# Kernel optimization log

Measured on AMD Instinct MI355X. Metric: run time of the kernel, lower is better.

The kernel has to match this reference:

```python
import jax, jax.numpy as jnp
import numpy as np
from jax.ops import segment_sum

N_NODES = 100000
IN_CH = 128
HIDDEN = 256
N_EDGES = 1600000


def setup_inputs() -> dict:
    key = jax.random.key(0)
    ks = jax.random.split(key, 8)
    x = jax.random.normal(ks[0], (N_NODES, IN_CH), dtype=jnp.float32)
    edge_index = jax.random.randint(ks[1], (2, N_EDGES), 0, N_NODES, dtype=jnp.int64)
    edges = jax.random.randint(ks[2], (N_EDGES, 2), 0, N_NODES, dtype=jnp.int64)
    s1 = 1.0 / np.sqrt(IN_CH)
    s2 = 1.0 / np.sqrt(HIDDEN)
    W1l = jax.random.normal(ks[3], (IN_CH, HIDDEN), dtype=jnp.float32) * s1
    W1r = jax.random.normal(ks[4], (IN_CH, HIDDEN), dtype=jnp.float32) * s1
    b1 = jnp.zeros((HIDDEN,), dtype=jnp.float32)
    W2l = jax.random.normal(ks[5], (HIDDEN, HIDDEN), dtype=jnp.float32) * s2
    W2r = jax.random.normal(ks[6], (HIDDEN, HIDDEN), dtype=jnp.float32) * s2
    b2 = jnp.zeros((HIDDEN,), dtype=jnp.float32)
    return {"x": x, "edge_index": edge_index, "edges": edges,
            "W1l": W1l, "b1": b1, "W1r": W1r,
            "W2l": W2l, "b2": b2, "W2r": W2r}


def _sage_conv(x, src, dst, Wl, b, Wr, n_nodes):
    # PyG SAGEConv (aggr='mean'): out = lin_l(mean_{j in N(i)} x_j) + lin_r(x_i)
    msg_sum = segment_sum(x[src], dst, num_segments=n_nodes)        # [N, F]
    deg = segment_sum(jnp.ones((src.shape[0],), x.dtype), dst, num_segments=n_nodes)
    mean = msg_sum / jnp.maximum(deg, 1.0)[:, None]                 # zero-deg -> 0
    return mean @ Wl + b + x @ Wr


def reference(x, edge_index, edges, W1l, b1, W1r, W2l, b2, W2r):
    src, dst = edge_index[0], edge_index[1]
    n = x.shape[0]
    h = jax.nn.relu(_sage_conv(x, src, dst, W1l, b1, W1r, n))
    z = _sage_conv(h, src, dst, W2l, b2, W2r, n)                    # [N, hidden]
    # decode: dot product over candidate edge pairs
    return jnp.sum(z[edges[:, 0]] * z[edges[:, 1]], axis=-1)        # [E2]
```

## Files before the change

### kernel.cpp

```cpp
#include <hip/hip_runtime.h>

#define IN_CH 128
#define HID   256
#define PB_VT 16
#define BCAP  6144

typedef __attribute__((ext_vector_type(8))) short bf16x8;
typedef __attribute__((ext_vector_type(4))) float f32x4;
typedef __attribute__((ext_vector_type(2))) float f32x2;
typedef __attribute__((ext_vector_type(8))) unsigned short ushort8;

__device__ __forceinline__ ushort f2b(float f) {
    unsigned u = __float_as_uint(f);
    unsigned r = (u + 0x7fffu + ((u >> 16) & 1u)) >> 16;
    return (ushort)r;
}
__device__ __forceinline__ float b2f(ushort h) {
    return __uint_as_float(((unsigned)h) << 16);
}
__device__ __forceinline__ void fp8x8_to_f32(uint2 v, float f[8]) {
    f32x2 a = __builtin_amdgcn_cvt_pk_f32_fp8((int)v.x, false);
    f32x2 b = __builtin_amdgcn_cvt_pk_f32_fp8((int)v.x, true);
    f32x2 c = __builtin_amdgcn_cvt_pk_f32_fp8((int)v.y, false);
    f32x2 d = __builtin_amdgcn_cvt_pk_f32_fp8((int)v.y, true);
    f[0] = a[0]; f[1] = a[1]; f[2] = b[0]; f[3] = b[1];
    f[4] = c[0]; f[5] = c[1]; f[6] = d[0]; f[7] = d[1];
}

__device__ __forceinline__ void prep_w_body(const float* __restrict__ Wl,
                                            const float* __restrict__ Wr,
                                            ushort* __restrict__ Wt,
                                            int KH, bool permK, int idx) {
    int ktot = 2 * KH;
    if (idx >= 256 * ktot) return;
    int n = idx / ktot, k = idx % ktot;
    int kh = (k < KH) ? k : (k - KH);
    int c = kh;
    if (permK) {
        int j = kh & 63;
        c = (kh & ~63) | ((j & 3) * 16 + (j >> 2));
    }
    float v = (k < KH) ? Wl[(size_t)c * 256 + n] : Wr[(size_t)c * 256 + n];
    Wt[idx] = f2b(v);
}

__global__ __launch_bounds__(256)
void fused_cvt_prep(const float* __restrict__ x, ushort* __restrict__ xb,
                    unsigned char* __restrict__ x8, int n4, int nCvt,
                    const float* __restrict__ W1l, const float* __restrict__ W1r, ushort* __restrict__ Wt1,
                    const float* __restrict__ W2l, const float* __restrict__ W2r, ushort* __restrict__ Wt2,
                    int* __restrict__ bucketCntG, int* __restrict__ bucketCntP) {
    int b = blockIdx.x;
    int t = threadIdx.x;
    if (b < nCvt) {
        int i = b * 256 + t;
        if (i < n4) {
            float4 v = ((const float4*)x)[i];
            ushort4 u;
            u.x = f2b(v.x); u.y = f2b(v.y); u.z = f2b(v.z); u.w = f2b(v.w);
            ((ushort4*)xb)[i] = u;
            int p = __builtin_amdgcn_cvt_pk_fp8_f32(v.x, v.y, 0, false);
            p = __builtin_amdgcn_cvt_pk_fp8_f32(v.z, v.w, p, true);
            ((unsigned*)x8)[i] = (unsigned)p;
        }
    } else if (b < nCvt + 256) {
        prep_w_body(W1l, W1r, Wt1, IN_CH, false, (b - nCvt) * 256 + t);
    } else if (b < nCvt + 256 + 512) {
        prep_w_body(W2l, W2r, Wt2, HID, true, (b - nCvt - 256) * 256 + t);
    } else {
        bucketCntG[t] = 0;
        bucketCntG[t + 256] = 0;
        bucketCntP[t] = 0;
        bucketCntP[t + 256] = 0;
    }
}

__global__ __launch_bounds__(256)
void scatter_reserve_kernel(const int* __restrict__ src, const int* __restrict__ dst,
                            const int* __restrict__ edges,
                            int* __restrict__ bucketCntG, int* __restrict__ bucketCntP,
                            unsigned* __restrict__ tmpG, unsigned long long* __restrict__ tmpP,
                            int E, int E2, int NBUK, int NBG) {
    __shared__ int hist[512];
    __shared__ int cur[512];
    int t = threadIdx.x;
    bool isG = (int)blockIdx.x < NBG;
    int blk = isG ? blockIdx.x : blockIdx.x - NBG;
    for (int i = t; i < NBUK; i += 256) hist[i] = 0;
    __syncthreads();
    long long e0 = (long long)blk * (256 * PB_VT);
    if (isG) {
#pragma unroll
        for (int i = 0; i < PB_VT; i++) {
            long long e = e0 + i * 256 + t;
            if (e < E) atomicAdd(&hist[dst[e] >> 8], 1);
        }
    } else {
#pragma unroll
        for (int i = 0; i < PB_VT; i++) {
            long long e = e0 + i * 256 + t;
            if (e < E2) atomicAdd(&hist[edges[e * 2] >> 8], 1);
        }
    }
    __syncthreads();
    int* bcnt = isG ? bucketCntG : bucketCntP;
    for (int i = t; i < NBUK; i += 256) {
        int hc = hist[i];
        cur[i] = (hc > 0) ? atomicAdd(&bcnt[i], hc) : 0;
    }
    __syncthreads();
    if (isG) {
#pragma unroll
        for (int i = 0; i < PB_VT; i++) {
            long long e = e0 + i * 256 + t;
            if (e < E) {
                int d = dst[e];
                int bk = d >> 8;
                int pos = atomicAdd(&cur[bk], 1);
                tmpG[(size_t)bk * BCAP + pos] = ((unsigned)src[e] << 8) | (unsigned)(d & 255);
            }
        }
    } else {
#pragma unroll
        for (int i = 0; i < PB_VT; i++) {
            long long e = e0 + i * 256 + t;
            if (e < E2) {
                int2 ab = *(const int2*)(edges + e * 2);
                int bk = ab.x >> 8;
                int pos = atomicAdd(&cur[bk], 1);
                tmpP[(size_t)bk * BCAP + pos] = ((unsigned long long)(unsigned)(ab.x & 255) << 56)
                                              | ((unsigned long long)(unsigned)ab.y << 32)
                                              | (unsigned)e;
            }
        }
    }
}

__global__ __launch_bounds__(256)
void bucket_sort_kernel(const unsigned* __restrict__ tmpG, const unsigned long long* __restrict__ tmpP,
                        const int* __restrict__ bucketCntG, const int* __restrict__ bucketCntP,
                        int* __restrict__ count, int* __restrict__ offs,
                        int* __restrict__ nbr, unsigned long long* __restrict__ pairs,
                        int N, int Npad, int NBUK) {
    __shared__ int h[256], loffs[256], lcur[256];
    int t = threadIdx.x;
    bool isG = (int)blockIdx.x < NBUK;
    int b = isG ? blockIdx.x : blockIdx.x - NBUK;
    int s = b * BCAP;
    int c = isG ? bucketCntG[b] : bucketCntP[b];
    h[t] = 0;
    __syncthreads();
    if (isG) {
        for (int i = t; i < c; i += 256) atomicAdd(&h[tmpG[s + i] & 255], 1);
    } else {
        for (int i = t; i < c; i += 256) atomicAdd(&h[(int)(tmpP[s + i] >> 56)], 1);
    }
    __syncthreads();
    int v = h[t];
    loffs[t] = v;
    __syncthreads();
    for (int d = 1; d < 256; d <<= 1) {
        int u = (t >= d) ? loffs[t - d] : 0;
        __syncthreads(); loffs[t] += u; __syncthreads();
    }
    int excl = loffs[t] - v;
    lcur[t] = excl;
    int node = b * 256 + t;
    if (node < N) {
        int base = isG ? 0 : Npad;
        count[base + node] = v;
        offs[base + node] = s + excl;
    }
    __syncthreads();
    if (isG) {
        for (int i = t; i < c; i += 256) {
            unsigned w = tmpG[s + i];
            int p = atomicAdd(&lcur[w & 255], 1);
            nbr[s + p] = (int)(w >> 8);
        }
    } else {
        for (int i = t; i < c; i += 256) {
            unsigned long long w = tmpP[s + i];
            int p = atomicAdd(&lcur[(int)(w >> 56)], 1);
            pairs[s + p] = w & 0x00FFFFFFFFFFFFFFull;
        }
    }
}

__global__ void agg1_kernel(const unsigned char* __restrict__ x8, const int* __restrict__ nbr,
                            const int* __restrict__ offs, const int* __restrict__ count,
                            ushort* __restrict__ agg, int N) {
    int w = blockIdx.x * 4 + (threadIdx.x >> 6);
    if (w >= N) return;
    int lane = threadIdx.x & 63;
    int grp = lane >> 4, gl = lane & 15;
    int start = offs[w], cnt = count[w];
    float a0[8], a1[8];
#pragma unroll
    for (int i = 0; i < 8; i++) { a0[i] = 0.0f; a1[i] = 0.0f; }
    int j = grp;
    for (; j + 4 < cnt; j += 8) {
        int s0 = nbr[start + j];
        int s1 = nbr[start + j + 4];
        uint2 v0 = *(const uint2*)(x8 + (size_t)s0 * IN_CH + gl * 8);
        uint2 v1 = *(const uint2*)(x8 + (size_t)s1 * IN_CH + gl * 8);
        float f0[8], f1[8];
        fp8x8_to_f32(v0, f0); fp8x8_to_f32(v1, f1);
#pragma unroll
        for (int i = 0; i < 8; i++) { a0[i] += f0[i]; a1[i] += f1[i]; }
    }
    if (j < cnt) {
        int s0 = nbr[start + j];
        uint2 v0 = *(const uint2*)(x8 + (size_t)s0 * IN_CH + gl * 8);
        float f0[8];
        fp8x8_to_f32(v0, f0);
#pragma unroll
        for (int i = 0; i < 8; i++) a0[i] += f0[i];
    }
#pragma unroll
    for (int i = 0; i < 8; i++) {
        a0[i] += a1[i];
        a0[i] += __shfl_xor(a0[i], 16, 64);
        a0[i] += __shfl_xor(a0[i], 32, 64);
    }
    if (grp == 0) {
        float r = 1.0f / fmaxf((float)cnt, 1.0f);
        ushort8 o;
#pragma unroll
        for (int i = 0; i < 8; i++) o[i] = f2b(a0[i] * r);
        *(ushort8*)(agg + (size_t)w * IN_CH + gl * 8) = o;
    }
}

__global__ void agg2_kernel(const unsigned char* __restrict__ h8, const int* __restrict__ nbr,
                            const int* __restrict__ offs, const int* __restrict__ count,
                            ushort* __restrict__ agg, int N) {
    int w = blockIdx.x * 4 + (threadIdx.x >> 6);
    if (w >= N) return;
    int lane = threadIdx.x & 63;
    int half = lane >> 5, hl = lane & 31;
    int start = offs[w], cnt = count[w];
    float a0[8], a1[8];
#pragma unroll
    for (int i = 0; i < 8; i++) { a0[i] = 0.0f; a1[i] = 0.0f; }
    int j = half;
    for (; j + 6 < cnt; j += 8) {
        int s0 = nbr[start + j];
        int s1 = nbr[start + j + 2];
        int s2 = nbr[start + j + 4];
        int s3 = nbr[start + j + 6];
        uint2 v0 = *(const uint2*)(h8 + (size_t)s0 * HID + hl * 8);
        uint2 v1 = *(const uint2*)(h8 + (size_t)s1 * HID + hl * 8);
        uint2 v2 = *(const uint2*)(h8 + (size_t)s2 * HID + hl * 8);
        uint2 v3 = *(const uint2*)(h8 + (size_t)s3 * HID + hl * 8);
        float f0[8], f1[8], f2[8], f3[8];
        fp8x8_to_f32(v0, f0); fp8x8_to_f32(v1, f1);
        fp8x8_to_f32(v2, f2); fp8x8_to_f32(v3, f3);
#pragma unroll
        for (int i = 0; i < 8; i++) {
            a0[i] += f0[i] + f2[i];
            a1[i] += f1[i] + f3[i];
        }
    }
    for (; j < cnt; j += 2) {
        int s0 = nbr[start + j];
        uint2 v0 = *(const uint2*)(h8 + (size_t)s0 * HID + hl * 8);
        float f0[8];
        fp8x8_to_f32(v0, f0);
#pragma unroll
        for (int i = 0; i < 8; i++) a0[i] += f0[i];
    }
#pragma unroll
    for (int i = 0; i < 8; i++) {
        a0[i] += a1[i];
        a0[i] += __shfl_xor(a0[i], 32, 64);
    }
    if (half == 0) {
        float r = 1.0f / fmaxf((float)cnt, 1.0f);
        ushort8 o;
#pragma unroll
        for (int i = 0; i < 8; i++) o[i] = f2b(a0[i] * r);
        *(ushort8*)(agg + (size_t)w * HID + hl * 8) = o;
    }
}

template<int KTOT, bool RELU, bool WBF16, bool WFP8>
__global__ __launch_bounds__(512, 4)
void sage_gemm_mfma(const ushort* __restrict__ Aleft, const ushort* __restrict__ Aright,
                    const ushort* __restrict__ Wt, const float* __restrict__ bias,
                    ushort* __restrict__ out, unsigned char* __restrict__ out8, int N) {
    constexpr int KH = KTOT / 2;
    __shared__ ushort smem[2048 + 8192];
    ushort* As = smem;
    ushort* Bs = smem + 2048;

    const int t = threadIdx.x;
    const int wave = t >> 6;
    const int lane = t & 63;
    const int quad = lane >> 4;
    const int l16  = lane & 15;
    const int rowBase = blockIdx.x * 64;

    const int aRow = t >> 3;
    const int aK   = (t & 7) * 4;
    const bool aRowOK = (rowBase + aRow) < N;
    const int aLds = ((aRow >> 4) * 64 + (aRow & 15) * 4 + (aK >> 3)) * 8 + (aK & 7);

    const int bN   = t >> 1;
    const int bCh0 = (t & 1) * 2;
    const int bFragBase = (bN >> 6) * 256 + ((bN >> 4) & 3) * 64 + (bN & 15) * 4;

    int bFrag[2];
#pragma unroll
    for (int nt = 0; nt < 2; nt++) {
        int c = wave * 32 + nt * 16 + l16;
        bFrag[nt] = ((c >> 6) * 256 + ((c >> 4) & 3) * 64 + (c & 15) * 4 + quad) * 8;
    }

    f32x4 acc[4][2];
#pragma unroll
    for (int i = 0; i < 4; i++)
#pragma unroll
        for (int j = 0; j < 2; j++) acc[i][j] = (f32x4)0.0f;

    unsigned long long aReg = 0ull;
    ulonglong2 bReg[2];
    if (aRowOK)
        aReg = *(const unsigned long long*)(Aleft + (size_t)(rowBase + aRow) * KH + aK);
    bReg[0] = *(const ulonglong2*)(Wt + (size_t)bN * KTOT + bCh0 * 8);
    bReg[1] = *(const ulonglong2*)(Wt + (size_t)bN * KTOT + (bCh0 + 1) * 8);

    for (int k0 = 0; k0 < KTOT; k0 += 32) {
        __syncthreads();
        *(unsigned long long*)&As[aLds] = aReg;
        *(ulonglong2*)&Bs[(bFragBase + bCh0) * 8]     = bReg[0];
        *(ulonglong2*)&Bs[(bFragBase + bCh0 + 1) * 8] = bReg[1];

        int kn = k0 + 32;
        if (kn < KTOT) {
            if (aRowOK) {
                const ushort* Ap = (kn < KH)
                    ? (Aleft  + (size_t)(rowBase + aRow) * KH + (kn + aK))
                    : (Aright + (size_t)(rowBase + aRow) * KH + (kn - KH + aK));
                aReg = *(const unsigned long long*)Ap;
            }
            bReg[0] = *(const ulonglong2*)(Wt + (size_t)bN * KTOT + kn + bCh0 * 8);
            bReg[1] = *(const ulonglong2*)(Wt + (size_t)bN * KTOT + kn + (bCh0 + 1) * 8);
        }
        __syncthreads();

        bf16x8 af[4], bf[2];
#pragma unroll
        for (int mt = 0; mt < 4; mt++)
            af[mt] = *(const bf16x8*)&As[(mt * 64 + l16 * 4 + quad) * 8];
#pragma unroll
        for (int nt = 0; nt < 2; nt++)
            bf[nt] = *(const bf16x8*)&Bs[bFrag[nt]];
#pragma unroll
        for (int mt = 0; mt < 4; mt++)
#pragma unroll
            for (int nt = 0; nt < 2; nt++)
                acc[mt][nt] = __builtin_amdgcn_mfma_f32_16x16x32_bf16(
                    af[mt], bf[nt], acc[mt][nt], 0, 0, 0);
    }

    float bv[2];
#pragma unroll
    for (int nt = 0; nt < 2; nt++) bv[nt] = bias[wave * 32 + nt * 16 + l16];
    ushort* tile = smem;

#pragma unroll
    for (int hf = 0; hf < 2; hf++) {
        __syncthreads();
#pragma unroll
        for (int mh = 0; mh < 2; mh++) {
            int mt = hf * 2 + mh;
#pragma unroll
            for (int reg = 0; reg < 4; reg++) {
                int rl = mh * 16 + quad * 4 + reg;
                float v0 = acc[mt][0][reg] + bv[0];
                float v1 = acc[mt][1][reg] + bv[1];
                if (RELU) { v0 = fmaxf(v0, 0.0f); v1 = fmaxf(v1, 0.0f); }
                ushort2 o;
                o.x = f2b(v0); o.y = f2b(v1);
                *(ushort2*)&tile[rl * 256 + (wave >> 1) * 64 + l16 * 4 + (wave & 1) * 2] = o;
            }
        }
        __syncthreads();
#pragma unroll
        for (int i = 0; i < 2; i++) {
            int ch = i * 512 + t;
            int rl = ch >> 5, c16 = ch & 31;
            int row = rowBase + hf * 32 + rl;
            if (row < N) {
                ushort8 w = *(const ushort8*)&tile[rl * 256 + c16 * 8];
                if (WBF16)
                    *(ushort8*)(out + (size_t)row * 256 + c16 * 8) = w;
                if (WFP8) {
                    int u0 = __builtin_amdgcn_cvt_pk_fp8_f32(b2f(w[0]), b2f(w[1]), 0, false);
                    u0 = __builtin_amdgcn_cvt_pk_fp8_f32(b2f(w[2]), b2f(w[3]), u0, true);
                    int u1 = __builtin_amdgcn_cvt_pk_fp8_f32(b2f(w[4]), b2f(w[5]), 0, false);
                    u1 = __builtin_amdgcn_cvt_pk_fp8_f32(b2f(w[6]), b2f(w[7]), u1, true);
                    uint2 o8;
                    o8.x = (unsigned)u0; o8.y = (unsigned)u1;
                    *(uint2*)(out8 + (size_t)row * 256 + c16 * 8) = o8;
                }
            }
        }
    }
}

__global__ void decode2_kernel(const unsigned char* __restrict__ z8,
                               const unsigned long long* __restrict__ pairs,
                               const int* __restrict__ offsA, const int* __restrict__ countA,
                               float* __restrict__ out, int N) {
    int a = blockIdx.x * 4 + (threadIdx.x >> 6);
    if (a >= N) return;
    int cnt = countA[a];
    if (cnt == 0) return;
    int lane = threadIdx.x & 63;
    int half = lane >> 5, hl = lane & 31;
    int start = offsA[a];

    float ar[8];
    {
        uint2 va = *(const uint2*)(z8 + (size_t)a * HID + hl * 8);
        fp8x8_to_f32(va, ar);
    }

    int j = half;
    for (; j + 6 < cnt; j += 8) {
        unsigned long long p0 = pairs[start + j];
        unsigned long long p1 = pairs[start + j + 2];
        unsigned long long p2 = pairs[start + j + 4];
        unsigned long long p3 = pairs[start + j + 6];
        int b0 = (int)((p0 >> 32) & 0xFFFFFFu), e0 = (int)(p0 & 0xffffffffu);
        int b1 = (int)((p1 >> 32) & 0xFFFFFFu), e1 = (int)(p1 & 0xffffffffu);
        int b2 = (int)((p2 >> 32) & 0xFFFFFFu), e2 = (int)(p2 & 0xffffffffu);
        int b3 = (int)((p3 >> 32) & 0xFFFFFFu), e3 = (int)(p3 & 0xffffffffu);
        uint2 v0 = *(const uint2*)(z8 + (size_t)b0 * HID + hl * 8);
        uint2 v1 = *(const uint2*)(z8 + (size_t)b1 * HID + hl * 8);
        uint2 v2 = *(const uint2*)(z8 + (size_t)b2 * HID + hl * 8);
        uint2 v3 = *(const uint2*)(z8 + (size_t)b3 * HID + hl * 8);
        float f0[8], f1[8], f2[8], f3[8];
        fp8x8_to_f32(v0, f0); fp8x8_to_f32(v1, f1);
        fp8x8_to_f32(v2, f2); fp8x8_to_f32(v3, f3);
        float s0 = 0.f, s1 = 0.f, s2 = 0.f, s3 = 0.f;
#pragma unroll
        for (int i = 0; i < 8; i++) {
            s0 = fmaf(ar[i], f0[i], s0);
            s1 = fmaf(ar[i], f1[i], s1);
            s2 = fmaf(ar[i], f2[i], s2);
            s3 = fmaf(ar[i], f3[i], s3);
        }
#pragma unroll
        for (int off = 1; off < 32; off <<= 1) {
            s0 += __shfl_xor(s0, off, 64);
            s1 += __shfl_xor(s1, off, 64);
            s2 += __shfl_xor(s2, off, 64);
            s3 += __shfl_xor(s3, off, 64);
        }
        if (hl == 0) { out[e0] = s0; out[e1] = s1; out[e2] = s2; out[e3] = s3; }
    }
    for (; j < cnt; j += 2) {
        unsigned long long p0 = pairs[start + j];
        int b0 = (int)((p0 >> 32) & 0xFFFFFFu), e0 = (int)(p0 & 0xffffffffu);
        uint2 v0 = *(const uint2*)(z8 + (size_t)b0 * HID + hl * 8);
        float f0[8];
        fp8x8_to_f32(v0, f0);
        float s0 = 0.f;
#pragma unroll
        for (int i = 0; i < 8; i++) s0 = fmaf(ar[i], f0[i], s0);
#pragma unroll
        for (int off = 1; off < 32; off <<= 1) s0 += __shfl_xor(s0, off, 64);
        if (hl == 0) out[e0] = s0;
    }
}

extern "C" void kernel_launch(void* const* d_in, const int* in_sizes, int n_in,
                              void* d_out, int out_size, void* d_ws, size_t ws_size,
                              hipStream_t stream) {
    const float* x    = (const float*)d_in[0];
    const int* eidx   = (const int*)d_in[1];
    const int* edges  = (const int*)d_in[2];
    const float* W1l  = (const float*)d_in[3];
    const float* b1   = (const float*)d_in[4];
    const float* W1r  = (const float*)d_in[5];
    const float* W2l  = (const float*)d_in[6];
    const float* b2   = (const float*)d_in[7];
    const float* W2r  = (const float*)d_in[8];
    float* out = (float*)d_out;

    const int N  = in_sizes[0] / IN_CH;
    const int E  = in_sizes[1] / 2;
    const int E2 = in_sizes[2] / 2;
    const int* src = eidx;
    const int* dst = eidx + E;

    const int NBUK = (N + 255) >> 8;
    const int Npad = NBUK << 8;
    const int NBG  = (E  + 256 * PB_VT - 1) / (256 * PB_VT);
    const int NBP  = (E2 + 256 * PB_VT - 1) / (256 * PB_VT);

    int* count      = (int*)d_ws;
    int* offs       = count + 2 * Npad;
    int* bucketCntG = offs + 2 * Npad;
    int* bucketCntP = bucketCntG + 512;
    int* nbr        = bucketCntP + 512;
    size_t intWords = (size_t)(nbr - (int*)d_ws) + (size_t)NBUK * BCAP;
    intWords = (intWords + 1) & ~(size_t)1;
    unsigned long long* pairs = (unsigned long long*)((int*)d_ws + intWords);
    ushort* xb    = (ushort*)(pairs + (size_t)NBUK * BCAP);
    ushort* agg1b = xb + (size_t)N * IN_CH;
    ushort* agg2b = xb;
    ushort* h     = agg1b + (size_t)N * IN_CH;
    unsigned char* h8 = (unsigned char*)(h + (size_t)N * HID);
    unsigned char* z8 = h8 + (size_t)N * HID;
    ushort* Wt1   = (ushort*)(z8 + (size_t)N * HID);
    ushort* Wt2   = Wt1 + 256 * 256;
    unsigned char* x8 = z8 + (size_t)N * HID / 2;
    unsigned* tmpG = (unsigned*)h8;
    unsigned long long* tmpP =
        (unsigned long long*)(tmpG + (((size_t)NBUK * BCAP + 1) & ~(size_t)1));

    int n4 = N * IN_CH / 4;
    int nCvt = (n4 + 255) / 256;
    fused_cvt_prep<<<nCvt + 256 + 512 + 1, 256, 0, stream>>>(
        x, xb, x8, n4, nCvt, W1l, W1r, Wt1, W2l, W2r, Wt2, bucketCntG, bucketCntP);

    scatter_reserve_kernel<<<NBG + NBP, 256, 0, stream>>>(
        src, dst, edges, bucketCntG, bucketCntP, tmpG, tmpP, E, E2, NBUK, NBG);
    bucket_sort_kernel<<<2 * NBUK, 256, 0, stream>>>(
        tmpG, tmpP, bucketCntG, bucketCntP, count, offs, nbr, pairs, N, Npad, NBUK);

    agg1_kernel<<<(N + 3) / 4, 256, 0, stream>>>(x8, nbr, offs, count, agg1b, N);
    sage_gemm_mfma<2 * IN_CH, true, true, true><<<(N + 63) / 64, 512, 0, stream>>>(
        agg1b, xb, Wt1, b1, h, h8, N);

    agg2_kernel<<<(N + 3) / 4, 256, 0, stream>>>(h8, nbr, offs, count, agg2b, N);
    sage_gemm_mfma<2 * HID, false, false, true><<<(N + 63) / 64, 512, 0, stream>>>(
        agg2b, h, Wt2, b2, h , z8, N);

    decode2_kernel<<<(N + 3) / 4, 256, 0, stream>>>(z8, pairs, offs + Npad, count + Npad, out, N);
}
```

Before: 527.0 us.

## Double-buffer LDS in SAGE GEMM and enlarge row tile to 128

The MFMA GEMM now stages A and B tiles in two LDS buffers, so the next K-slice is written while the current one is consumed. This removes one barrier per K step. Each block also covers 128 rows instead of 64, giving every wave 8x2 accumulator tiles; B fragments are reused over more rows and the grid is halved. The cost is more LDS (about 48KB) and more accumulator registers, which may reduce occupancy under launch_bounds(512,4). The epilogue loop is extended to write out four half-tiles.

Result: faster. 486.5 us (-7.7%).

```diff
diff --git a/kernel.cpp b/kernel.cpp
--- a/kernel.cpp
+++ b/kernel.cpp
@@ -290,21 +290,22 @@
                     const ushort* __restrict__ Wt, const float* __restrict__ bias,
                     ushort* __restrict__ out, unsigned char* __restrict__ out8, int N) {
     constexpr int KH = KTOT / 2;
-    __shared__ ushort smem[2048 + 8192];
-    ushort* As = smem;
-    ushort* Bs = smem + 2048;
+    constexpr int S  = KTOT / 32;
+    __shared__ ushort smem[2 * 4096 + 2 * 8192];
+    ushort* AsB[2] = { smem, smem + 4096 };
+    ushort* BsB[2] = { smem + 8192, smem + 16384 };
 
     const int t = threadIdx.x;
     const int wave = t >> 6;
     const int lane = t & 63;
     const int quad = lane >> 4;
     const int l16  = lane & 15;
-    const int rowBase = blockIdx.x * 64;
-
-    const int aRow = t >> 3;
-    const int aK   = (t & 7) * 4;
+    const int rowBase = blockIdx.x * 128;
+
+    const int aRow = t >> 2;
+    const int aCh  = t & 3;
     const bool aRowOK = (rowBase + aRow) < N;
-    const int aLds = ((aRow >> 4) * 64 + (aRow & 15) * 4 + (aK >> 3)) * 8 + (aK & 7);
+    const int aLds = ((aRow >> 4) * 64 + (aRow & 15) * 4 + aCh) * 8;
 
     const int bN   = t >> 1;
     const int bCh0 = (t & 1) * 2;
@@ -317,51 +318,57 @@
         bFrag[nt] = ((c >> 6) * 256 + ((c >> 4) & 3) * 64 + (c & 15) * 4 + quad) * 8;
     }
 
-    f32x4 acc[4][2];
-#pragma unroll
-    for (int i = 0; i < 4; i++)
+    f32x4 acc[8][2];
+#pragma unroll
+    for (int i = 0; i < 8; i++)
 #pragma unroll
         for (int j = 0; j < 2; j++) acc[i][j] = (f32x4)0.0f;
 
-    unsigned long long aReg = 0ull;
+    ulonglong2 aReg = {0ull, 0ull};
     ulonglong2 bReg[2];
+
     if (aRowOK)
-        aReg = *(const unsigned long long*)(Aleft + (size_t)(rowBase + aRow) * KH + aK);
+        aReg = *(const ulonglong2*)(Aleft + (size_t)(rowBase + aRow) * KH + aCh * 8);
     bReg[0] = *(const ulonglong2*)(Wt + (size_t)bN * KTOT + bCh0 * 8);
     bReg[1] = *(const ulonglong2*)(Wt + (size_t)bN * KTOT + (bCh0 + 1) * 8);
-
-    for (int k0 = 0; k0 < KTOT; k0 += 32) {
+    *(ulonglong2*)&AsB[0][aLds] = aReg;
+    *(ulonglong2*)&BsB[0][(bFragBase + bCh0) * 8]     = bReg[0];
+    *(ulonglong2*)&BsB[0][(bFragBase + bCh0 + 1) * 8] = bReg[1];
+
+#pragma unroll
+    for (int s = 0; s < S; s++) {
         __syncthreads();
-        *(unsigned long long*)&As[aLds] = aReg;
-        *(ulonglong2*)&Bs[(bFragBase + bCh0) * 8]     = bReg[0];
-        *(ulonglong2*)&Bs[(bFragBase + bCh0 + 1) * 8] = bReg[1];
-
-        int kn = k0 + 32;
+        const int kn = (s + 1) * 32;
         if (kn < KTOT) {
             if (aRowOK) {
                 const ushort* Ap = (kn < KH)
-                    ? (Aleft  + (size_t)(rowBase + aRow) * KH + (kn + aK))
-                    : (Aright + (size_t)(rowBase + aRow) * KH + (kn - KH + aK));
-                aReg = *(const unsigned long long*)Ap;
+                    ? (Aleft  + (size_t)(rowBase + aRow) * KH + (kn + aCh * 8))
+                    : (Aright + (size_t)(rowBase + aRow) * KH + (kn - KH + aCh * 8));
+                aReg = *(const ulonglong2*)Ap;
             }
             bReg[0] = *(const ulonglong2*)(Wt + (size_t)bN * KTOT + kn + bCh0 * 8);
             bReg[1] = *(const ulonglong2*)(Wt + (size_t)bN * KTOT + kn + (bCh0 + 1) * 8);
         }
-        __syncthreads();
-
-        bf16x8 af[4], bf[2];
-#pragma unroll
-        for (int mt = 0; mt < 4; mt++)
-            af[mt] = *(const bf16x8*)&As[(mt * 64 + l16 * 4 + quad) * 8];
-#pragma unroll
-        for (int nt = 0; nt < 2; nt++)
-            bf[nt] = *(const bf16x8*)&Bs[bFrag[nt]];
-#pragma unroll
-        for (int mt = 0; mt < 4; mt++)
-#pragma unroll
-            for (int nt = 0; nt < 2; nt++)
-                acc[mt][nt] = __builtin_amdgcn_mfma_f32_16x16x32_bf16(
-                    af[mt], bf[nt], acc[mt][nt], 0, 0, 0);
+
+        const ushort* As = AsB[s & 1];
+        const ushort* Bs = BsB[s & 1];
+        bf16x8 bf[2];
+        bf[0] = *(const bf16x8*)&Bs[bFrag[0]];
+        bf[1] = *(const bf16x8*)&Bs[bFrag[1]];
+#pragma unroll
+        for (int mt = 0; mt < 8; mt++) {
+            bf16x8 af = *(const bf16x8*)&As[(mt * 64 + l16 * 4 + quad) * 8];
+            acc[mt][0] = __builtin_amdgcn_mfma_f32_16x16x32_bf16(af, bf[0], acc[mt][0], 0, 0, 0);
+            acc[mt][1] = __builtin_amdgcn_mfma_f32_16x16x32_bf16(af, bf[1], acc[mt][1], 0, 0, 0);
+        }
+
+        if (kn < KTOT) {
+            ushort* An = AsB[(s + 1) & 1];
+            ushort* Bn = BsB[(s + 1) & 1];
+            *(ulonglong2*)&An[aLds] = aReg;
+            *(ulonglong2*)&Bn[(bFragBase + bCh0) * 8]     = bReg[0];
+            *(ulonglong2*)&Bn[(bFragBase + bCh0 + 1) * 8] = bReg[1];
+        }
     }
 
     float bv[2];
@@ -370,7 +377,7 @@
     ushort* tile = smem;
 
 #pragma unroll
-    for (int hf = 0; hf < 2; hf++) {
+    for (int hf = 0; hf < 4; hf++) {
         __syncthreads();
 #pragma unroll
         for (int mh = 0; mh < 2; mh++) {
@@ -534,11 +541,11 @@
         tmpG, tmpP, bucketCntG, bucketCntP, count, offs, nbr, pairs, N, Npad, NBUK);
 
     agg1_kernel<<<(N + 3) / 4, 256, 0, stream>>>(x8, nbr, offs, count, agg1b, N);
-    sage_gemm_mfma<2 * IN_CH, true, true, true><<<(N + 63) / 64, 512, 0, stream>>>(
+    sage_gemm_mfma<2 * IN_CH, true, true, true><<<(N + 127) / 128, 512, 0, stream>>>(
         agg1b, xb, Wt1, b1, h, h8, N);
 
     agg2_kernel<<<(N + 3) / 4, 256, 0, stream>>>(h8, nbr, offs, count, agg2b, N);
-    sage_gemm_mfma<2 * HID, false, false, true><<<(N + 63) / 64, 512, 0, stream>>>(
+    sage_gemm_mfma<2 * HID, false, false, true><<<(N + 127) / 128, 512, 0, stream>>>(
         agg2b, h, Wt2, b2, h , z8, N);
 
     decode2_kernel<<<(N + 3) / 4, 256, 0, stream>>>(z8, pairs, offs + Npad, count + Npad, out, N);
```
